# Kernel tuning notes

Hardware: AMD Instinct MI355X
Metric: run time of the kernel (lower is better)

The kernel has to match this reference:

```python
import jax, jax.numpy as jnp
import numpy as np

B, W, L = 16, 128, 20
SIGMA = 2.0


def _make_kernel(L, sigma):
    i = jnp.arange(L, dtype=jnp.float32)
    d = i[:, None] - i[None, :]
    return jnp.exp(-(d * d) / (sigma * sigma))  # [L, L]


def setup_inputs() -> dict:
    key = jax.random.key(0)
    k1, _ = jax.random.split(key)
    anonymized_nodes = jax.random.randint(k1, (B, W, L), 0, L)
    walk_masks = jnp.ones((B, W, L), dtype=jnp.float32)
    kernel = _make_kernel(L, SIGMA)  # registered buffer in the torch module
    return {"anonymized_nodes": anonymized_nodes, "walk_masks": walk_masks, "kernel": kernel}


def reference(anonymized_nodes, walk_masks, kernel):
    # match[b,r,s,i,j] = (a[b,r,i] == a[b,s,j]) & mask[b,r,i] & mask[b,s,j]
    match = anonymized_nodes[:, :, None, :, None] == anonymized_nodes[:, None, :, None, :]
    mbool = walk_masks > 0
    match = match & mbool[:, :, None, :, None] & mbool[:, None, :, None, :]
    # C[b,r,s] = sum_{i,j} match[b,r,s,i,j] * kernel[i,j]
    coocc = jnp.einsum('brsij,ij->brs', match.astype(jnp.float32), kernel)
    valid = walk_masks.sum(axis=-1)  # [B, W]
    norm = valid[:, :, None] * valid[:, None, :] + 1e-8
    return coocc / norm
```

## Files before the change

### kernel.cpp

```cpp
#include <hip/hip_runtime.h>


#define BB 16
#define WW 128
#define LL 20

__global__ __launch_bounds__(128) void coocc_kernel(
    const int*   __restrict__ a,
    const float* __restrict__ mask,
    const float* __restrict__ kern,
    float*       __restrict__ out)
{
    __shared__ float h[LL * LL];
    __shared__ int   am_r[LL];
    __shared__ float vr_sh;

    const int t   = threadIdx.x;
    const int bid = blockIdx.x;
    const int b   = bid >> 7;

    const int base = (b * WW + t) * LL;
    int4   av[5];
    float4 mv[5];
    const int4*   ap = (const int4*)  (a    + base);
    const float4* mp = (const float4*)(mask + base);
    #pragma unroll
    for (int q = 0; q < 5; ++q) { av[q] = ap[q]; mv[q] = mp[q]; }

    float m_own = 0.f;
    if (t < LL) {
        const int   va = a[bid * LL + t];
        const float mm = mask[bid * LL + t];
        am_r[t] = (mm > 0.f) ? va : -1;
        m_own = mm;
    }
    if (t < 64) {
        float v = m_own;
        #pragma unroll
        for (int off = 32; off; off >>= 1) v += __shfl_xor(v, off, 64);
        if (t == 0) vr_sh = v;
    }

    if (t < 100) ((float4*)h)[t] = make_float4(0.f, 0.f, 0.f, 0.f);
    __syncthreads();

    #pragma unroll
    for (int rep = 0; rep < 4; ++rep) {
        const int e = t + rep * 128;
        if (e < LL * LL) {
            const int   i  = e / LL;
            const int   j  = e - i * LL;
            const int   v  = am_r[i];
            const float kv = kern[e];
            if (v >= 0) atomicAdd(&h[v * LL + j], kv);
        }
    }
    __syncthreads();

    const float valid_r = vr_sh;
    float acc = 0.f, valid_s = 0.f;
    #pragma unroll
    for (int q = 0; q < 5; ++q) {
        const int   aa[4] = {av[q].x, av[q].y, av[q].z, av[q].w};
        const float mm[4] = {mv[q].x, mv[q].y, mv[q].z, mv[q].w};
        #pragma unroll
        for (int k = 0; k < 4; ++k) {
            const int j = q * 4 + k;
            valid_s += mm[k];
            const float hv = h[aa[k] * LL + j];
            acc += (mm[k] > 0.f) ? hv : 0.f;
        }
    }
    out[bid * WW + t] = acc / (valid_r * valid_s + 1e-8f);
}

extern "C" void kernel_launch(void* const* d_in, const int* in_sizes, int n_in,
                              void* d_out, int out_size, void* d_ws, size_t ws_size,
                              hipStream_t stream) {
    const int*   a    = (const int*)  d_in[0];
    const float* mask = (const float*)d_in[1];
    const float* kern = (const float*)d_in[2];
    float*       out  = (float*)d_out;

    coocc_kernel<<<BB * WW, 128, 0, stream>>>(a, mask, kern, out);
}
```

Measured before the change: 63.86 us.

## Stage whole batch walk codes in padded LDS with coalesced loads

Each block now loads the entire batch's anonymized nodes and masks with coalesced int4/float4 reads. It writes masked codes into a padded shared array (stride 21) with a sentinel row for masked positions, and computes per-walk valid counts via shared atomics. The histogram and final gather then read codes from LDS without per-element mask checks, and the kernel values are prefetched before the first barrier. This targets strided per-thread global loads and LDS bank conflicts, at the cost of more shared memory, an extra barrier and many shared atomics for the valid counts.

```diff
diff --git a/kernel.cpp b/kernel.cpp
--- a/kernel.cpp
+++ b/kernel.cpp
@@ -4,6 +4,8 @@
 #define BB 16
 #define WW 128
 #define LL 20
+#define PL 21
+#define HR 21
 
 __global__ __launch_bounds__(128) void coocc_kernel(
     const int*   __restrict__ a,
@@ -11,67 +13,76 @@
     const float* __restrict__ kern,
     float*       __restrict__ out)
 {
-    __shared__ float h[LL * LL];
-    __shared__ int   am_r[LL];
-    __shared__ float vr_sh;
+    __shared__ int   code [WW * PL];
+    __shared__ float h    [HR * PL];
+    __shared__ float valid[WW];
 
     const int t   = threadIdx.x;
     const int bid = blockIdx.x;
     const int b   = bid >> 7;
+    const int r   = bid & (WW - 1);
 
-    const int base = (b * WW + t) * LL;
+    const int4*   ap = (const int4*)  (a    + b * (WW * LL));
+    const float4* mp = (const float4*)(mask + b * (WW * LL));
     int4   av[5];
     float4 mv[5];
-    const int4*   ap = (const int4*)  (a    + base);
-    const float4* mp = (const float4*)(mask + base);
     #pragma unroll
-    for (int q = 0; q < 5; ++q) { av[q] = ap[q]; mv[q] = mp[q]; }
-
-    float m_own = 0.f;
-    if (t < LL) {
-        const int   va = a[bid * LL + t];
-        const float mm = mask[bid * LL + t];
-        am_r[t] = (mm > 0.f) ? va : -1;
-        m_own = mm;
+    for (int q = 0; q < 5; ++q) {
+        av[q] = ap[q * 128 + t];
+        mv[q] = mp[q * 128 + t];
     }
-    if (t < 64) {
-        float v = m_own;
-        #pragma unroll
-        for (int off = 32; off; off >>= 1) v += __shfl_xor(v, off, 64);
-        if (t == 0) vr_sh = v;
+    float kv[4];
+    #pragma unroll
+    for (int q = 0; q < 4; ++q) {
+        const int e = t + q * 128;
+        kv[q] = (e < LL * LL) ? kern[e] : 0.f;
     }
 
-    if (t < 100) ((float4*)h)[t] = make_float4(0.f, 0.f, 0.f, 0.f);
+    #pragma unroll
+    for (int q = 0; q < 4; ++q) {
+        const int e = t + q * 128;
+        if (e < HR * PL) h[e] = 0.f;
+    }
+    valid[t] = 0.f;
     __syncthreads();
 
     #pragma unroll
-    for (int rep = 0; rep < 4; ++rep) {
-        const int e = t + rep * 128;
-        if (e < LL * LL) {
-            const int   i  = e / LL;
-            const int   j  = e - i * LL;
-            const int   v  = am_r[i];
-            const float kv = kern[e];
-            if (v >= 0) atomicAdd(&h[v * LL + j], kv);
+    for (int q = 0; q < 5; ++q) {
+        const int   c0    = (q * 128 + t) * 4;
+        const int   aa[4] = {av[q].x, av[q].y, av[q].z, av[q].w};
+        const float mm[4] = {mv[q].x, mv[q].y, mv[q].z, mv[q].w};
+        #pragma unroll
+        for (int k = 0; k < 4; ++k) {
+            const int e   = c0 + k;
+            const int row = e / LL;
+            const int col = e - row * LL;
+            code[row * PL + col] = (mm[k] > 0.f) ? aa[k] : LL;
+            atomicAdd(&valid[row], mm[k]);
         }
     }
     __syncthreads();
 
-    const float valid_r = vr_sh;
-    float acc = 0.f, valid_s = 0.f;
     #pragma unroll
-    for (int q = 0; q < 5; ++q) {
-        const int   aa[4] = {av[q].x, av[q].y, av[q].z, av[q].w};
-        const float mm[4] = {mv[q].x, mv[q].y, mv[q].z, mv[q].w};
-        #pragma unroll
-        for (int k = 0; k < 4; ++k) {
-            const int j = q * 4 + k;
-            valid_s += mm[k];
-            const float hv = h[aa[k] * LL + j];
-            acc += (mm[k] > 0.f) ? hv : 0.f;
+    for (int q = 0; q < 4; ++q) {
+        const int e = t + q * 128;
+        if (e < LL * LL) {
+            const int i = e / LL;
+            const int j = e - i * LL;
+            const int v = code[r * PL + i];
+            if (v < LL) atomicAdd(&h[v * PL + j], kv[q]);
         }
     }
-    out[bid * WW + t] = acc / (valid_r * valid_s + 1e-8f);
+    __syncthreads();
+
+    float acc = 0.f;
+    #pragma unroll
+    for (int j = 0; j < LL; ++j) {
+        const int c = code[t * PL + j];
+        acc += h[c * PL + j];
+    }
+    const float vr = valid[r];
+    const float vs = valid[t];
+    out[bid * WW + t] = acc / (vr * vs + 1e-8f);
 }
 
 extern "C" void kernel_launch(void* const* d_in, const int* in_sizes, int n_in,
```

After: 94.85 us. 48.5% more time.
